# Kernel tuning notes

Hardware: AMD Instinct MI355X
Metric: run time of the kernel (lower is better)

Reference implementation:

```python
import jax, jax.numpy as jnp
import numpy as np

BN_EPS = 1e-5


def _bn(h, gamma, beta):
    # torch BatchNorm1d training-mode forward: biased batch variance
    mu = h.mean(axis=0)
    var = h.var(axis=0)
    return (h - mu) * jax.lax.rsqrt(var + BN_EPS) * gamma + beta


def setup_inputs() -> dict:
    N, E, H = 100000, 1600000, 128
    HID = 2 * H  # get_torch_mlp hidden_channels = 2*out_channels = 256
    key = jax.random.key(0)
    ks = jax.random.split(key, 8)
    s_lin = 1.0 / np.sqrt(H)
    s_mlp = 1.0 / np.sqrt(2 * H)
    return {
        "x": jax.random.normal(ks[0], (N, H), dtype=jnp.float32),
        "edge_index": jax.random.randint(ks[1], (2, E), 0, N, dtype=jnp.int64),
        "lin_w": jax.random.normal(ks[2], (2 * H, H), dtype=jnp.float32) * s_lin,
        "lin_b": jnp.zeros((2 * H,), dtype=jnp.float32),
        "eps": jnp.zeros((), dtype=jnp.float32),
        "w1": jax.random.normal(ks[3], (HID, 2 * H), dtype=jnp.float32) * s_mlp,
        "g1": jnp.ones((HID,), dtype=jnp.float32),
        "b1": jnp.zeros((HID,), dtype=jnp.float32),
        "w2": jax.random.normal(ks[4], (HID, HID), dtype=jnp.float32) * (1.0 / np.sqrt(HID)),
        "g2": jnp.ones((HID,), dtype=jnp.float32),
        "b2": jnp.zeros((HID,), dtype=jnp.float32),
        "w3": jax.random.normal(ks[5], (H, HID), dtype=jnp.float32) * (1.0 / np.sqrt(HID)),
        "b3": jnp.zeros((H,), dtype=jnp.float32),
    }


def reference(x, edge_index, lin_w, lin_b, eps, w1, g1, b1, w2, g2, b2, w3, b3):
    N = x.shape[0]
    dst, src = edge_index[0], edge_index[1]
    # transfer1(atoms, G): irregular gather of neighbor rows + scatter-add,
    # duplicated across the two order-1 linmap channel blocks -> [N, 2H]
    agg = jax.ops.segment_sum(x[src], dst, num_segments=N)
    x_transfer = jnp.concatenate([agg, agg], axis=-1)
    # linmaps1 on singleton domains: [broadcast(sum)=x, id=x] -> [N, 2H]
    x_linmaps = jnp.concatenate([x, x], axis=-1)
    x_lin = x @ lin_w.T + lin_b
    h = x_lin + (1.0 + eps) * x_linmaps + x_transfer  # stack([...]).sum(0)
    # MLP: Linear(no bias) -> BN -> ReLU -> Linear(no bias) -> BN -> ReLU -> Linear(bias)
    h = jax.nn.relu(_bn(h @ w1.T, g1, b1))
    h = jax.nn.relu(_bn(h @ w2.T, g2, b2))
    h = h @ w3.T + b3
    return h  # rows of the output ptensors1 (same atoms)
```

## Files before the change

### kernel.cpp

```cpp
#include <hip/hip_runtime.h>
#include <cstdint>
#include <cstddef>

typedef __bf16 bf16_t;
typedef __bf16 bf16x8 __attribute__((ext_vector_type(8)));
typedef float f32x4 __attribute__((ext_vector_type(4)));

#define GLOBAL_AS __attribute__((address_space(1)))
#define LDS_AS    __attribute__((address_space(3)))

__device__ __forceinline__ void glds16(const void* g, void* l) {
    __builtin_amdgcn_global_load_lds((const GLOBAL_AS void*)g, (LDS_AS void*)l, 16, 0, 0);
}

__global__ void conv_k(const float* __restrict__ in, bf16_t* __restrict__ out, int n8) {
    int id = blockIdx.x * 256 + threadIdx.x;
    if (id >= n8) return;
    const float4* p = (const float4*)in;
    float4 a = p[2 * id], b = p[2 * id + 1];
    bf16x8 o;
    o[0] = (bf16_t)a.x; o[1] = (bf16_t)a.y; o[2] = (bf16_t)a.z; o[3] = (bf16_t)a.w;
    o[4] = (bf16_t)b.x; o[5] = (bf16_t)b.y; o[6] = (bf16_t)b.z; o[7] = (bf16_t)b.w;
    *(bf16x8*)(out + (size_t)id * 8) = o;
}

__global__ void conv_x_k(const float* __restrict__ in, bf16_t* __restrict__ ha, int n8) {
    int id = blockIdx.x * 256 + threadIdx.x;
    if (id >= n8) return;
    const float4* p = (const float4*)in;
    float4 a = p[2 * id], b = p[2 * id + 1];
    bf16x8 o;
    o[0] = (bf16_t)a.x; o[1] = (bf16_t)a.y; o[2] = (bf16_t)a.z; o[3] = (bf16_t)a.w;
    o[4] = (bf16_t)b.x; o[5] = (bf16_t)b.y; o[6] = (bf16_t)b.z; o[7] = (bf16_t)b.w;
    int row = id >> 4, ch = id & 15;
    *(bf16x8*)(ha + (size_t)row * 256 + ch * 8) = o;
}

__global__ void wcomb_k(const float* __restrict__ w1, const float* __restrict__ lin_w,
                        const float* __restrict__ lin_b, const float* __restrict__ eps_p,
                        bf16_t* __restrict__ wc, float* __restrict__ bcomb) {
    __shared__ float red[256];
    int c = blockIdx.x, t = threadIdx.x;
    const float* w1row = w1 + c * 256;
    float onepe = 1.f + *eps_p;
    float v;
    if (t < 128) {
        float acc = 0.f;
        for (int j = 0; j < 256; j++) acc += w1row[j] * lin_w[j * 128 + t];
        v = acc + onepe * (w1row[t] + w1row[t + 128]);
    } else {
        int m = t - 128;
        v = w1row[m] + w1row[t];
    }
    wc[c * 256 + t] = (bf16_t)v;
    red[t] = w1row[t] * lin_b[t];
    __syncthreads();
    for (int off = 128; off > 0; off >>= 1) {
        if (t < off) red[t] += red[t + off];
        __syncthreads();
    }
    if (t == 0) bcomb[c] = red[0];
}

__global__ void detect_k(const int* __restrict__ ei, int* __restrict__ flag) {
    int v = ei[2 * threadIdx.x + 1];
    if (v != 0) atomicOr(flag, 1);
}

#define CHUNK 8192

__global__ __launch_bounds__(256) void bhist_k(const void* __restrict__ ei, const int* __restrict__ flag,
                                               int E, int* __restrict__ bcnt) {
    __shared__ int cnt[1024];
    int t = threadIdx.x;
    for (int b = t; b < 1024; b += 256) cnt[b] = 0;
    __syncthreads();
    int base = blockIdx.x * CHUNK;
    int i32 = *flag;
#pragma unroll 4
    for (int i = 0; i < CHUNK / 256; i++) {
        int e = base + t + 256 * i;
        if (e < E) {
            int dst = i32 ? ((const int*)ei)[e] : (int)((const long long*)ei)[e];
            atomicAdd(&cnt[dst >> 7], 1);
        }
    }
    __syncthreads();
    for (int b = t; b < 1024; b += 256)
        if (cnt[b]) atomicAdd(&bcnt[b], cnt[b]);
}

__global__ __launch_bounds__(1024) void bscan_k(const int* __restrict__ bcnt, int* __restrict__ boffs,
                                                int* __restrict__ gcur, int* __restrict__ offs,
                                                int NBK, int N, int E) {
    __shared__ int lds[1024];
    int t = threadIdx.x;
    int v = (t < NBK) ? bcnt[t] : 0;
    lds[t] = v;
    __syncthreads();
    for (int off = 1; off < 1024; off <<= 1) {
        int add = (t >= off) ? lds[t - off] : 0;
        __syncthreads();
        lds[t] += add;
        __syncthreads();
    }
    if (t < NBK) {
        int excl = lds[t] - v;
        boffs[t] = excl;
        gcur[t] = excl;
    }
    if (t == 0) { boffs[NBK] = E; offs[N] = E; }
}

__global__ __launch_bounds__(256) void binfill_k(const void* __restrict__ ei, const int* __restrict__ flag,
                                                 int E, int NBK, int* __restrict__ gcur,
                                                 unsigned* __restrict__ pairs) {
    __shared__ int cnt[1024];
    __shared__ int pref[1024];
    __shared__ int cur[1024];
    __shared__ int gbase[1024];
    __shared__ int red[256];
    __shared__ unsigned slot[CHUNK];
    __shared__ unsigned short sbk[CHUNK];
    int t = threadIdx.x;
    int base = blockIdx.x * CHUNK;
    int chunk_n = E - base; if (chunk_n > CHUNK) chunk_n = CHUNK;
    int i32 = *flag;
    for (int b = t; b < 1024; b += 256) cnt[b] = 0;
    __syncthreads();
#pragma unroll 4
    for (int i = 0; i < CHUNK / 256; i++) {
        int e = base + t + 256 * i;
        if (e < E) {
            int dst = i32 ? ((const int*)ei)[e] : (int)((const long long*)ei)[e];
            atomicAdd(&cnt[dst >> 7], 1);
        }
    }
    __syncthreads();
    int t4 = t * 4;
    int c0 = cnt[t4], c1 = cnt[t4 + 1], c2 = cnt[t4 + 2], c3 = cnt[t4 + 3];
    int s = c0 + c1 + c2 + c3;
    red[t] = s;
    __syncthreads();
    for (int off = 1; off < 256; off <<= 1) {
        int add = (t >= off) ? red[t - off] : 0;
        __syncthreads();
        red[t] += add;
        __syncthreads();
    }
    int run = red[t] - s;
    pref[t4] = run; cur[t4] = run; run += c0;
    pref[t4 + 1] = run; cur[t4 + 1] = run; run += c1;
    pref[t4 + 2] = run; cur[t4 + 2] = run; run += c2;
    pref[t4 + 3] = run; cur[t4 + 3] = run;
    __syncthreads();
#pragma unroll 4
    for (int i = 0; i < CHUNK / 256; i++) {
        int e = base + t + 256 * i;
        if (e < E) {
            int dst, src;
            if (i32) { dst = ((const int*)ei)[e]; src = ((const int*)ei)[E + e]; }
            else     { dst = (int)((const long long*)ei)[e]; src = (int)((const long long*)ei)[E + e]; }
            int b = dst >> 7;
            int p = atomicAdd(&cur[b], 1);
            slot[p] = ((unsigned)(dst & 127) << 20) | (unsigned)src;
            sbk[p] = (unsigned short)b;
        }
    }
    __syncthreads();
    for (int b = t; b < 1024; b += 256) {
        int c = (b + 1 < 1024) ? (pref[b + 1] - pref[b]) : (chunk_n - pref[b]);
        if (b < NBK && c > 0) gbase[b] = atomicAdd(&gcur[b], c);
    }
    __syncthreads();
    for (int i = t; i < chunk_n; i += 256) {
        int bk = sbk[i];
        pairs[gbase[bk] + (i - pref[bk])] = slot[i];
    }
}

__global__ __launch_bounds__(256) void bsort2_k(const unsigned* __restrict__ pairs,
                                                const int* __restrict__ boffs,
                                                int* __restrict__ offs,
                                                int* __restrict__ csr, int N) {
    __shared__ int cnt[128], pref[128], cur[128];
    int t = threadIdx.x;
    int b = blockIdx.x;
    int s = boffs[b], e = boffs[b + 1];
    if (t < 128) cnt[t] = 0;
    __syncthreads();
    for (int i = s + t; i < e; i += 256)
        atomicAdd(&cnt[pairs[i] >> 20], 1);
    __syncthreads();
    if (t < 128) pref[t] = cnt[t];
    __syncthreads();
    for (int off = 1; off < 128; off <<= 1) {
        int v = 0;
        if (t < 128 && t >= off) v = pref[t - off];
        __syncthreads();
        if (t < 128) pref[t] += v;
        __syncthreads();
    }
    if (t < 128) {
        int ex = pref[t] - cnt[t];
        cur[t] = ex;
        int node = b * 128 + t;
        if (node < N) offs[node] = s + ex;
    }
    __syncthreads();
    for (int i = s + t; i < e; i += 256) {
        unsigned u = pairs[i];
        int dl = (int)(u >> 20);
        int p = atomicAdd(&cur[dl], 1);
        csr[s + p] = (int)(u & 0xFFFFFu);
    }
}

__global__ __launch_bounds__(256) void gather_k(bf16_t* __restrict__ ha, const int* __restrict__ offs,
                                                const int* __restrict__ csr, int N) {
    int w = (blockIdx.x * 256 + threadIdx.x) >> 6;
    if (w >= N) return;
    int lane = threadIdx.x & 63;
    int g = lane >> 4, l15 = lane & 15;
    int s = offs[w], e = offs[w + 1];
    float acc[8] = {0.f, 0.f, 0.f, 0.f, 0.f, 0.f, 0.f, 0.f};
    float acc2[8] = {0.f, 0.f, 0.f, 0.f, 0.f, 0.f, 0.f, 0.f};
    int i = s + g;
    bool h0 = i < e, h1 = i + 4 < e;
    int p0 = h0 ? csr[i] : 0;
    int p1 = h1 ? csr[i + 4] : 0;
    while (h1) {
        int ni = i + 8;
        bool nh0 = ni < e, nh1 = ni + 4 < e;
        int np0 = nh0 ? csr[ni] : 0;
        int np1 = nh1 ? csr[ni + 4] : 0;
        bf16x8 v0 = *(const bf16x8*)(ha + (size_t)p0 * 256 + l15 * 8);
        bf16x8 v1 = *(const bf16x8*)(ha + (size_t)p1 * 256 + l15 * 8);
#pragma unroll
        for (int j = 0; j < 8; j++) { acc[j] += (float)v0[j]; acc2[j] += (float)v1[j]; }
        i = ni; p0 = np0; p1 = np1; h0 = nh0; h1 = nh1;
    }
    if (h0) {
        bf16x8 v0 = *(const bf16x8*)(ha + (size_t)p0 * 256 + l15 * 8);
#pragma unroll
        for (int j = 0; j < 8; j++) acc[j] += (float)v0[j];
    }
#pragma unroll
    for (int j = 0; j < 8; j++) {
        acc[j] += acc2[j];
        acc[j] += __shfl_xor(acc[j], 16);
        acc[j] += __shfl_xor(acc[j], 32);
    }
    if (g == 0) {
        bf16x8 o;
#pragma unroll
        for (int j = 0; j < 8; j++) o[j] = (bf16_t)acc[j];
        *(bf16x8*)(ha + (size_t)w * 256 + 128 + l15 * 8) = o;
    }
}

template<int NCOLTOT, bool BNIN, bool STATS, bool FINAL, bool BIAS>
__global__ __launch_bounds__(512, 4) void gemm_q(
    const bf16_t* __restrict__ A, const bf16_t* __restrict__ W,
    const float2* __restrict__ scsh2,
    float* __restrict__ sums, float* __restrict__ sqs,
    const float* __restrict__ bias,
    bf16_t* __restrict__ Obf, float* __restrict__ Of, int N, int ntiles, int shift)
{
    __shared__ __align__(16) char smemW[32768];
    __shared__ __align__(16) char smemA[32768];

    const int tid = threadIdx.x;
    const int lane = tid & 63, wid = tid >> 6;
    const int l15 = lane & 15, l4 = lane >> 4;
    const int rowg = wid & 1, colg = wid >> 1;
    const int tstride = 1 << shift;
    const int colq = (int)blockIdx.x >> shift;
    const int rb = (int)blockIdx.x & (tstride - 1);

#pragma unroll
    for (int it = 0; it < 4; it++) {
        int d = (it * 512 + tid) * 16;
        int col = d >> 9, koff = d & 511;
        int ksw = koff ^ ((col & 7) << 4);
        glds16((const char*)W + (size_t)(colq * 64 + col) * 512 + ksw, smemW + d);
    }

    auto stageA = [&](int t) {
        size_t rowbase = (size_t)t * 64;
#pragma unroll
        for (int it = 0; it < 4; it++) {
            int d = (it * 512 + tid) * 16;
            int row = d >> 9, koff = d & 511;
            int ksw = koff ^ ((row & 7) << 4);
            glds16((const char*)A + (rowbase + row) * 512 + ksw, smemA + d);
        }
    };

    float2 sslr[32];
    if constexpr (BNIN) {
#pragma unroll
        for (int it = 0; it < 4; it++) {
            int d = (it * 512 + tid) * 16;
            int row = d >> 9;
            int k0 = ((d & 511) ^ ((row & 7) << 4)) >> 1;
#pragma unroll
            for (int i = 0; i < 8; i++) sslr[it * 8 + i] = scsh2[k0 + i];
        }
    }

    auto transformA = [&]() {
#pragma unroll
        for (int it = 0; it < 4; it++) {
            int d = (it * 512 + tid) * 16;
            bf16x8 v = *(const bf16x8*)(smemA + d);
            bf16x8 o;
#pragma unroll
            for (int i = 0; i < 8; i++) {
                float2 ss = sslr[it * 8 + i];
                o[i] = (bf16_t)fmaxf((float)v[i] * ss.x + ss.y, 0.f);
            }
            *(bf16x8*)(smemA + d) = o;
        }
    };

    const int colw = colq * 64 + colg * 16 + l15;
    float bbv = 0.f;
    if constexpr (BIAS || FINAL) bbv = bias[colw];
    float sA = 0.f, qA = 0.f;

    f32x4 acc[2];

    auto compute = [&]() {
        acc[0] = f32x4{0.f, 0.f, 0.f, 0.f};
        acc[1] = f32x4{0.f, 0.f, 0.f, 0.f};
        const int col = colg * 16 + l15;
        const int wsw = (col & 7) << 4;
#pragma unroll
        for (int c = 0; c < 8; c++) {
            const int koff = c * 64 + l4 * 16;
            bf16x8 a0, a1;
            {
                int row = rowg * 32 + l15;
                a0 = *(const bf16x8*)(smemA + row * 512 + (koff ^ ((row & 7) << 4)));
                row += 16;
                a1 = *(const bf16x8*)(smemA + row * 512 + (koff ^ ((row & 7) << 4)));
            }
            const bf16x8 b = *(const bf16x8*)(smemW + col * 512 + (koff ^ wsw));
            acc[0] = __builtin_amdgcn_mfma_f32_16x16x32_bf16(a0, b, acc[0], 0, 0, 0);
            acc[1] = __builtin_amdgcn_mfma_f32_16x16x32_bf16(a1, b, acc[1], 0, 0, 0);
        }
    };

    auto epilogue = [&](int t) {
        const int rows0 = t * 64 + rowg * 32;
#pragma unroll
        for (int fr = 0; fr < 2; fr++) {
            int rb0 = rows0 + fr * 16 + l4 * 4;
            f32x4 av = acc[fr];
#pragma unroll
            for (int i = 0; i < 4; i++) {
                int r = rb0 + i;
                if constexpr (FINAL) {
                    if (r < N) Of[(size_t)r * NCOLTOT + colw] = av[i] + bbv;
                } else {
                    float v = av[i];
                    if constexpr (BIAS) v += bbv;
                    bf16_t hv = (bf16_t)v;
                    if (r < N) Obf[(size_t)r * 256 + colw] = hv;
                    if constexpr (STATS) {
                        float vv = (r < N) ? (float)hv : 0.f;
                        sA += vv; qA += vv * vv;
                    }
                }
            }
        }
    };

    int t = rb;
    if (t < ntiles) stageA(t);
    __syncthreads();
    if constexpr (BNIN) {
        if (t < ntiles) transformA();
        __syncthreads();
    }

    while (t < ntiles) {
        compute();
        __syncthreads();
        int tn = t + tstride;
        if (tn < ntiles) stageA(tn);
        epilogue(t);
        __syncthreads();
        if constexpr (BNIN) {
            if (tn < ntiles) transformA();
            __syncthreads();
        }
        t = tn;
    }

    if constexpr (STATS) {
        sA += __shfl_xor(sA, 16); sA += __shfl_xor(sA, 32);
        qA += __shfl_xor(qA, 16); qA += __shfl_xor(qA, 32);
        if (lane < 16) {
            atomicAdd(&sums[colw], sA);
            atomicAdd(&sqs[colw], qA);
        }
    }
}

__global__ void finalize_k(const float* __restrict__ sum, const float* __restrict__ sq,
                           const float* __restrict__ g, const float* __restrict__ b,
                           float2* __restrict__ scsh2, float invN) {
    int t = threadIdx.x;
    float mean = sum[t] * invN;
    float var = sq[t] * invN - mean * mean;
    float s = g[t] * rsqrtf(var + 1e-5f);
    scsh2[t] = make_float2(s, b[t] - mean * s);
}

extern "C" void kernel_launch(void* const* d_in, const int* in_sizes, int n_in,
                              void* d_out, int out_size, void* d_ws, size_t ws_size,
                              hipStream_t stream)
{
    const int N = in_sizes[0] / 128;
    const int E = in_sizes[1] / 2;
    const float* x     = (const float*)d_in[0];
    const void*  ei    = d_in[1];
    const float* lin_w = (const float*)d_in[2];
    const float* lin_b = (const float*)d_in[3];
    const float* eps   = (const float*)d_in[4];
    const float* w1    = (const float*)d_in[5];
    const float* g1    = (const float*)d_in[6];
    const float* b1    = (const float*)d_in[7];
    const float* w2    = (const float*)d_in[8];
    const float* g2    = (const float*)d_in[9];
    const float* b2    = (const float*)d_in[10];
    const float* w3    = (const float*)d_in[11];
    const float* b3    = (const float*)d_in[12];
    float* out = (float*)d_out;

    char* ws = (char*)d_ws;
    size_t o = 0;
    auto alloc = [&](size_t bytes) -> char* {
        char* p = ws + o;
        o = (o + bytes + 255) & ~(size_t)255;
        return p;
    };
    bf16_t*   ha    = (bf16_t*)alloc((size_t)N * 256 * 2);
    bf16_t*   hb    = (bf16_t*)alloc((size_t)N * 256 * 2);
    bf16_t*   wcb   = (bf16_t*)alloc((size_t)256 * 256 * 2);
    bf16_t*   w2b   = (bf16_t*)alloc((size_t)256 * 256 * 2);
    bf16_t*   w3b   = (bf16_t*)alloc((size_t)128 * 256 * 2);
    float*    bcomb = (float*)alloc(256 * 4);
    float*    stats = (float*)alloc(4 * 256 * 4);
    float2*   scsh1 = (float2*)alloc(256 * 8);
    float2*   scsh2 = (float2*)alloc(256 * 8);
    int*      bcnt  = (int*)alloc(1024 * 4);
    int*      boffs = (int*)alloc(1025 * 4);
    int*      gcur  = (int*)alloc(1024 * 4);
    int*      offs  = (int*)alloc((size_t)(N + 1) * 4);
    unsigned* pairs = (unsigned*)alloc((size_t)E * 4);
    int*      csr   = (int*)alloc((size_t)E * 4);
    int*      flag  = (int*)alloc(4);

    const int NBK = (N + 127) >> 7;

    hipMemsetAsync(bcnt, 0, 1024 * 4, stream);
    hipMemsetAsync(stats, 0, 4 * 256 * 4, stream);
    hipMemsetAsync(flag, 0, 4, stream);

    int nx8 = N * 16;
    conv_x_k<<<(nx8 + 255) / 256, 256, 0, stream>>>(x, ha, nx8);
    wcomb_k<<<256, 256, 0, stream>>>(w1, lin_w, lin_b, eps, wcb, bcomb);
    conv_k<<<32, 256, 0, stream>>>(w2, w2b, 8192);
    conv_k<<<16, 256, 0, stream>>>(w3, w3b, 4096);

    const int nch = (E + CHUNK - 1) / CHUNK;
    detect_k<<<1, 256, 0, stream>>>((const int*)ei, flag);
    bhist_k<<<nch, 256, 0, stream>>>(ei, flag, E, bcnt);
    bscan_k<<<1, 1024, 0, stream>>>(bcnt, boffs, gcur, offs, NBK, N, E);
    binfill_k<<<nch, 256, 0, stream>>>(ei, flag, E, NBK, gcur, pairs);
    bsort2_k<<<NBK, 256, 0, stream>>>(pairs, boffs, offs, csr, N);
    gather_k<<<(N + 3) / 4, 256, 0, stream>>>(ha, offs, csr, N);

    const int nt64 = (N + 63) / 64;
    gemm_q<256, false, true, false, true><<<512, 512, 0, stream>>>(
        ha, wcb, nullptr, stats + 0, stats + 256, bcomb, hb, nullptr, N, nt64, 7);
    finalize_k<<<1, 256, 0, stream>>>(stats + 0, stats + 256, g1, b1, scsh1, 1.f / (float)N);
    gemm_q<256, true, true, false, false><<<512, 512, 0, stream>>>(
        hb, w2b, scsh1, stats + 512, stats + 768, nullptr, ha, nullptr, N, nt64, 7);
    finalize_k<<<1, 256, 0, stream>>>(stats + 512, stats + 768, g2, b2, scsh2, 1.f / (float)N);
    gemm_q<128, true, false, true, true><<<512, 512, 0, stream>>>(
        ha, w3b, scsh2, nullptr, nullptr, b3, nullptr, out, N, nt64, 8);
}
```

Baseline: 242.5 us.

## Prefetch GEMM A tiles into registers and apply BN before LDS write

The GEMM A-tile staging moves from direct global-to-LDS loads to register prefetch. The next tile is loaded while the current one computes, the BN scale/shift and ReLU are applied in registers, and the result is written swizzled into LDS. This cuts the LDS read-modify-write pass and one barrier per tile. BN scale/shift are packed as a bf16 pair in one 32-bit word to save registers, which lowers their precision. The CSR now stores precomputed byte offsets so the gather skips the multiply.

```diff
diff --git a/kernel.cpp b/kernel.cpp
--- a/kernel.cpp
+++ b/kernel.cpp
@@ -11,6 +11,10 @@
 
 __device__ __forceinline__ void glds16(const void* g, void* l) {
     __builtin_amdgcn_global_load_lds((const GLOBAL_AS void*)g, (LDS_AS void*)l, 16, 0, 0);
+}
+
+__device__ __forceinline__ float bf2f(unsigned short u) {
+    union { unsigned int i; float f; } c; c.i = ((unsigned int)u) << 16; return c.f;
 }
 
 __global__ void conv_k(const float* __restrict__ in, bf16_t* __restrict__ out, int n8) {
@@ -212,7 +216,7 @@
         unsigned u = pairs[i];
         int dl = (int)(u >> 20);
         int p = atomicAdd(&cur[dl], 1);
-        csr[s + p] = (int)(u & 0xFFFFFu);
+        csr[s + p] = (int)((u & 0xFFFFFu) << 9);
     }
 }
 
@@ -234,14 +238,14 @@
         bool nh0 = ni < e, nh1 = ni + 4 < e;
         int np0 = nh0 ? csr[ni] : 0;
         int np1 = nh1 ? csr[ni + 4] : 0;
-        bf16x8 v0 = *(const bf16x8*)(ha + (size_t)p0 * 256 + l15 * 8);
-        bf16x8 v1 = *(const bf16x8*)(ha + (size_t)p1 * 256 + l15 * 8);
+        bf16x8 v0 = *(const bf16x8*)((const char*)ha + (size_t)(unsigned)p0 + l15 * 16);
+        bf16x8 v1 = *(const bf16x8*)((const char*)ha + (size_t)(unsigned)p1 + l15 * 16);
 #pragma unroll
         for (int j = 0; j < 8; j++) { acc[j] += (float)v0[j]; acc2[j] += (float)v1[j]; }
         i = ni; p0 = np0; p1 = np1; h0 = nh0; h1 = nh1;
     }
     if (h0) {
-        bf16x8 v0 = *(const bf16x8*)(ha + (size_t)p0 * 256 + l15 * 8);
+        bf16x8 v0 = *(const bf16x8*)((const char*)ha + (size_t)(unsigned)p0 + l15 * 16);
 #pragma unroll
         for (int j = 0; j < 8; j++) acc[j] += (float)v0[j];
     }
@@ -262,7 +266,7 @@
 template<int NCOLTOT, bool BNIN, bool STATS, bool FINAL, bool BIAS>
 __global__ __launch_bounds__(512, 4) void gemm_q(
     const bf16_t* __restrict__ A, const bf16_t* __restrict__ W,
-    const float2* __restrict__ scsh2,
+    const unsigned* __restrict__ scshp,
     float* __restrict__ sums, float* __restrict__ sqs,
     const float* __restrict__ bias,
     bf16_t* __restrict__ Obf, float* __restrict__ Of, int N, int ntiles, int shift)
@@ -286,41 +290,47 @@
         glds16((const char*)W + (size_t)(colq * 64 + col) * 512 + ksw, smemW + d);
     }
 
-    auto stageA = [&](int t) {
+    unsigned sslp[32];
+    if constexpr (BNIN) {
+#pragma unroll
+        for (int it = 0; it < 4; it++) {
+            int d = (it * 512 + tid) * 16;
+            int k0 = (d & 511) >> 1;
+#pragma unroll
+            for (int i = 0; i < 8; i++) sslp[it * 8 + i] = scshp[k0 + i];
+        }
+    }
+
+    bf16x8 rA[4];
+    auto loadA = [&](int t) {
         size_t rowbase = (size_t)t * 64;
 #pragma unroll
         for (int it = 0; it < 4; it++) {
             int d = (it * 512 + tid) * 16;
             int row = d >> 9, koff = d & 511;
-            int ksw = koff ^ ((row & 7) << 4);
-            glds16((const char*)A + (rowbase + row) * 512 + ksw, smemA + d);
+            rA[it] = *(const bf16x8*)((const char*)A + (rowbase + row) * 512 + koff);
         }
     };
-
-    float2 sslr[32];
-    if constexpr (BNIN) {
+    auto transformR = [&]() {
+#pragma unroll
+        for (int it = 0; it < 4; it++) {
+            bf16x8 v = rA[it], o;
+#pragma unroll
+            for (int i = 0; i < 8; i++) {
+                unsigned p = sslp[it * 8 + i];
+                float sc = bf2f((unsigned short)(p & 0xffff));
+                float sh = bf2f((unsigned short)(p >> 16));
+                o[i] = (bf16_t)fmaxf((float)v[i] * sc + sh, 0.f);
+            }
+            rA[it] = o;
+        }
+    };
+    auto writeA = [&]() {
 #pragma unroll
         for (int it = 0; it < 4; it++) {
             int d = (it * 512 + tid) * 16;
-            int row = d >> 9;
-            int k0 = ((d & 511) ^ ((row & 7) << 4)) >> 1;
-#pragma unroll
-            for (int i = 0; i < 8; i++) sslr[it * 8 + i] = scsh2[k0 + i];
-        }
-    }
-
-    auto transformA = [&]() {
-#pragma unroll
-        for (int it = 0; it < 4; it++) {
-            int d = (it * 512 + tid) * 16;
-            bf16x8 v = *(const bf16x8*)(smemA + d);
-            bf16x8 o;
-#pragma unroll
-            for (int i = 0; i < 8; i++) {
-                float2 ss = sslr[it * 8 + i];
-                o[i] = (bf16_t)fmaxf((float)v[i] * ss.x + ss.y, 0.f);
-            }
-            *(bf16x8*)(smemA + d) = o;
+            int row = d >> 9, koff = d & 511;
+            *(bf16x8*)(smemA + row * 512 + (koff ^ ((row & 7) << 4))) = rA[it];
         }
     };
 
@@ -378,24 +388,24 @@
     };
 
     int t = rb;
-    if (t < ntiles) stageA(t);
-    __syncthreads();
-    if constexpr (BNIN) {
-        if (t < ntiles) transformA();
-        __syncthreads();
-    }
+    if (t < ntiles) {
+        loadA(t);
+        if constexpr (BNIN) transformR();
+        writeA();
+    }
+    __syncthreads();
 
     while (t < ntiles) {
+        int tn = t + tstride;
+        if (tn < ntiles) loadA(tn);
         compute();
-        __syncthreads();
-        int tn = t + tstride;
-        if (tn < ntiles) stageA(tn);
         epilogue(t);
         __syncthreads();
-        if constexpr (BNIN) {
-            if (tn < ntiles) transformA();
-            __syncthreads();
-        }
+        if (tn < ntiles) {
+            if constexpr (BNIN) transformR();
+            writeA();
+        }
+        __syncthreads();
         t = tn;
     }
 
@@ -411,12 +421,15 @@
 
 __global__ void finalize_k(const float* __restrict__ sum, const float* __restrict__ sq,
                            const float* __restrict__ g, const float* __restrict__ b,
-                           float2* __restrict__ scsh2, float invN) {
+                           unsigned* __restrict__ scshp, float invN) {
     int t = threadIdx.x;
     float mean = sum[t] * invN;
     float var = sq[t] * invN - mean * mean;
     float s = g[t] * rsqrtf(var + 1e-5f);
-    scsh2[t] = make_float2(s, b[t] - mean * s);
+    float sh = b[t] - mean * s;
+    unsigned short us = __builtin_bit_cast(unsigned short, (bf16_t)s);
+    unsigned short uh = __builtin_bit_cast(unsigned short, (bf16_t)sh);
+    scshp[t] = (unsigned)us | ((unsigned)uh << 16);
 }
 
 extern "C" void kernel_launch(void* const* d_in, const int* in_sizes, int n_in,
@@ -454,8 +467,8 @@
     bf16_t*   w3b   = (bf16_t*)alloc((size_t)128 * 256 * 2);
     float*    bcomb = (float*)alloc(256 * 4);
     float*    stats = (float*)alloc(4 * 256 * 4);
-    float2*   scsh1 = (float2*)alloc(256 * 8);
-    float2*   scsh2 = (float2*)alloc(256 * 8);
+    unsigned* scshp1 = (unsigned*)alloc(256 * 4);
+    unsigned* scshp2 = (unsigned*)alloc(256 * 4);
     int*      bcnt  = (int*)alloc(1024 * 4);
     int*      boffs = (int*)alloc(1025 * 4);
     int*      gcur  = (int*)alloc(1024 * 4);
@@ -487,10 +500,10 @@
     const int nt64 = (N + 63) / 64;
     gemm_q<256, false, true, false, true><<<512, 512, 0, stream>>>(
         ha, wcb, nullptr, stats + 0, stats + 256, bcomb, hb, nullptr, N, nt64, 7);
-    finalize_k<<<1, 256, 0, stream>>>(stats + 0, stats + 256, g1, b1, scsh1, 1.f / (float)N);
+    finalize_k<<<1, 256, 0, stream>>>(stats + 0, stats + 256, g1, b1, scshp1, 1.f / (float)N);
     gemm_q<256, true, true, false, false><<<512, 512, 0, stream>>>(
-        hb, w2b, scsh1, stats + 512, stats + 768, nullptr, ha, nullptr, N, nt64, 7);
-    finalize_k<<<1, 256, 0, stream>>>(stats + 512, stats + 768, g2, b2, scsh2, 1.f / (float)N);
+        hb, w2b, scshp1, stats + 512, stats + 768, nullptr, ha, nullptr, N, nt64, 7);
+    finalize_k<<<1, 256, 0, stream>>>(stats + 512, stats + 768, g2, b2, scshp2, 1.f / (float)N);
     gemm_q<128, true, false, true, true><<<512, 512, 0, stream>>>(
-        ha, w3b, scsh2, nullptr, nullptr, b3, nullptr, out, N, nt64, 8);
-}
+        ha, w3b, scshp2, nullptr, nullptr, b3, nullptr, out, N, nt64, 8);
+}
```

New measurement: 251.5 us. 1.04x slower.
